# Kernel tuning notes

Measured on AMD Instinct MI355X. Metric: run time of the kernel, lower is better.

The kernel has to match this reference:

```python
import jax, jax.numpy as jnp
import numpy as np

B, D, S, O = 32768, 1024, 64, 4  # batch, feature_dim, n_subjects, n_outputs


def setup_inputs() -> dict:
    key = jax.random.key(0)
    kx, ks, kw, kb = jax.random.split(key, 4)
    x = jax.random.normal(kx, (B, D), dtype=jnp.float32)          # backbone features
    subject_ids = jax.random.randint(ks, (B,), 0, S)              # per-sample head id
    W = jax.random.normal(kw, (S, D, O), dtype=jnp.float32) / np.float32(np.sqrt(D))
    b = jax.random.normal(kb, (S, O), dtype=jnp.float32) * 0.01
    return {"x": x, "subject_ids": subject_ids, "W": W, "b": b}


def reference(x, subject_ids, W, b):
    # Vectorized form of the per-subject loop:
    #   for sid in unique(subject_ids): outputs[idxs] = heads[sid](features[idxs])
    # Each head is Linear(D, O): out[i] = x[i] @ W[sid[i]] + b[sid[i]].
    Wg = jnp.take(W, subject_ids, axis=0)   # [B, D, O] gathered per-sample weights
    bg = jnp.take(b, subject_ids, axis=0)   # [B, O]
    return jnp.einsum('bd,bdo->bo', x, Wg) + bg
```

## Files before the change

### kernel.cpp

```cpp
#include <hip/hip_runtime.h>

constexpr int B = 32768;
constexpr int D = 1024;
constexpr int S = 64;
constexpr int O = 4;


constexpr int CHUNKS      = 32;
constexpr int CHUNK       = B / CHUNKS;
constexpr int SEG         = CHUNK / 4;
constexpr int MAIN_BLOCKS = S * CHUNKS;

__global__ __launch_bounds__(256, 4) void main_kernel(
    const float* __restrict__ x,
    const int*   __restrict__ sid,
    const float* __restrict__ W,
    const float* __restrict__ bias,
    float*       __restrict__ out)
{
    __shared__ int list[4][SEG];

    const int lane = threadIdx.x & 63;
    const int wave = threadIdx.x >> 6;
    const int s    = blockIdx.x >> 5;
    const int c    = blockIdx.x & 31;
    const int q    = lane >> 4;

    const int seg = c * CHUNK + wave * SEG;
    int cnt = 0;
    #pragma unroll
    for (int r = 0; r < 4; ++r) {
        const int i = seg + r * 64 + lane;
        const bool m = (sid[i] == s);
        const unsigned long long mask = __ballot(m);
        const int rank = __popcll(mask & ((1ull << lane) - 1ull));
        if (m) list[wave][cnt + rank] = i;
        cnt += __popcll(mask);
    }

    float4 wreg[16];
    {
        const float4* Wp = (const float4*)(W + (size_t)s * (D * O));
        #pragma unroll
        for (int jj = 0; jj < 4; ++jj)
            #pragma unroll
            for (int cc = 0; cc < 4; ++cc)
                wreg[4 * jj + cc] = Wp[256 * jj + 4 * lane + cc];
    }
    const float bb = bias[(s << 2) + q];

    if (cnt == 0) return;

#define LOADX(XB, ROW)                                                         \
    {                                                                          \
        const float4* xr = (const float4*)(x + ((size_t)(ROW) << 10));         \
        _Pragma("unroll")                                                      \
        for (int j = 0; j < 4; ++j) XB[j] = xr[64 * j + lane];                 \
    }

#define COMPUTE(XC, ROW)                                                       \
    {                                                                          \
        float a0 = 0.f, a1 = 0.f, a2 = 0.f, a3 = 0.f;                          \
        _Pragma("unroll")                                                      \
        for (int j = 0; j < 4; ++j) {                                          \
            const float4 xv = XC[j];                                           \
            const float4 w0 = wreg[4 * j + 0];                                 \
            const float4 w1 = wreg[4 * j + 1];                                 \
            const float4 w2 = wreg[4 * j + 2];                                 \
            const float4 w3 = wreg[4 * j + 3];                                 \
            a0 += xv.x * w0.x; a1 += xv.x * w0.y;                              \
            a2 += xv.x * w0.z; a3 += xv.x * w0.w;                              \
            a0 += xv.y * w1.x; a1 += xv.y * w1.y;                              \
            a2 += xv.y * w1.z; a3 += xv.y * w1.w;                              \
            a0 += xv.z * w2.x; a1 += xv.z * w2.y;                              \
            a2 += xv.z * w2.z; a3 += xv.z * w2.w;                              \
            a0 += xv.w * w3.x; a1 += xv.w * w3.y;                              \
            a2 += xv.w * w3.z; a3 += xv.w * w3.w;                              \
        }                                                                      \
        _Pragma("unroll")                                                      \
        for (int m = 16; m <= 32; m <<= 1) {                                   \
            a0 += __shfl_xor(a0, m, 64);                                       \
            a1 += __shfl_xor(a1, m, 64);                                       \
            a2 += __shfl_xor(a2, m, 64);                                       \
            a3 += __shfl_xor(a3, m, 64);                                       \
        }                                                                      \
        float v = (q == 0) ? a0 : (q == 1) ? a1 : (q == 2) ? a2 : a3;          \
        _Pragma("unroll")                                                      \
        for (int m = 1; m <= 8; m <<= 1)                                       \
            v += __shfl_xor(v, m, 64);                                         \
        if ((lane & 15) == 0)                                                  \
            out[((size_t)(ROW) << 2) + q] = v + bb;                            \
    }

    float4 xbA[4], xbB[4];
    int rowA = __builtin_amdgcn_readfirstlane(list[wave][0]);
    LOADX(xbA, rowA)

    int k = 0;
    #pragma unroll 1
    while (k + 2 <= cnt) {
        const int rowB = __builtin_amdgcn_readfirstlane(list[wave][k + 1]);
        LOADX(xbB, rowB)
        COMPUTE(xbA, rowA)
        if (k + 2 < cnt) {
            const int rowN = __builtin_amdgcn_readfirstlane(list[wave][k + 2]);
            LOADX(xbA, rowN)
            COMPUTE(xbB, rowB)
            rowA = rowN;
        } else {
            COMPUTE(xbB, rowB)
        }
        k += 2;
    }
    if (k < cnt)
        COMPUTE(xbA, rowA)

#undef LOADX
#undef COMPUTE
}

extern "C" void kernel_launch(void* const* d_in, const int* in_sizes, int n_in,
                              void* d_out, int out_size, void* d_ws, size_t ws_size,
                              hipStream_t stream) {
    const float* x    = (const float*)d_in[0];
    const int*   sid  = (const int*)d_in[1];
    const float* W    = (const float*)d_in[2];
    const float* bias = (const float*)d_in[3];
    float* out = (float*)d_out;

    main_kernel<<<MAIN_BLOCKS, 256, 0, stream>>>(x, sid, W, bias, out);
}
```

Before: 230.8 us.

## Stage transposed head weights in shared memory and halve chunk count

Each block now loads the subject's weight matrix once into LDS in an output-major transposed layout and reads it per row, instead of holding 16 float4 weights in registers per lane. The batch is split into 16 chunks instead of 32, so each wave scans twice as many ids and processes more matched rows. Occupancy is pinned via waves_per_eu. This aims to cut register pressure and redundant W loads, at the cost of added LDS reads per row and a block barrier.

Measured after the change: 206.2 us. 10.6% less time.

```diff
diff --git a/kernel.cpp b/kernel.cpp
--- a/kernel.cpp
+++ b/kernel.cpp
@@ -6,30 +6,47 @@
 constexpr int O = 4;
 
 
-constexpr int CHUNKS      = 32;
+constexpr int CHUNKS      = 16;
 constexpr int CHUNK       = B / CHUNKS;
 constexpr int SEG         = CHUNK / 4;
 constexpr int MAIN_BLOCKS = S * CHUNKS;
 
-__global__ __launch_bounds__(256, 4) void main_kernel(
+__global__ __launch_bounds__(256)
+__attribute__((amdgpu_waves_per_eu(4, 4)))
+void main_kernel(
     const float* __restrict__ x,
     const int*   __restrict__ sid,
     const float* __restrict__ W,
     const float* __restrict__ bias,
     float*       __restrict__ out)
 {
-    __shared__ int list[4][SEG];
+    __shared__ float Wt[O * D];
+    __shared__ int   list[4][SEG];
 
-    const int lane = threadIdx.x & 63;
-    const int wave = threadIdx.x >> 6;
-    const int s    = blockIdx.x >> 5;
-    const int c    = blockIdx.x & 31;
+    const int t    = threadIdx.x;
+    const int lane = t & 63;
+    const int wave = t >> 6;
+    const int s    = blockIdx.x >> 4;
+    const int c    = blockIdx.x & 15;
     const int q    = lane >> 4;
+
+    {
+        const float4* Wp = (const float4*)(W + (size_t)s * (D * O));
+        #pragma unroll
+        for (int r = 0; r < 4; ++r) {
+            const int d = r * 256 + t;
+            const float4 w4 = Wp[d];
+            Wt[0 * D + d] = w4.x;
+            Wt[1 * D + d] = w4.y;
+            Wt[2 * D + d] = w4.z;
+            Wt[3 * D + d] = w4.w;
+        }
+    }
 
     const int seg = c * CHUNK + wave * SEG;
     int cnt = 0;
     #pragma unroll
-    for (int r = 0; r < 4; ++r) {
+    for (int r = 0; r < 8; ++r) {
         const int i = seg + r * 64 + lane;
         const bool m = (sid[i] == s);
         const unsigned long long mask = __ballot(m);
@@ -38,18 +55,11 @@
         cnt += __popcll(mask);
     }
 
-    float4 wreg[16];
-    {
-        const float4* Wp = (const float4*)(W + (size_t)s * (D * O));
-        #pragma unroll
-        for (int jj = 0; jj < 4; ++jj)
-            #pragma unroll
-            for (int cc = 0; cc < 4; ++cc)
-                wreg[4 * jj + cc] = Wp[256 * jj + 4 * lane + cc];
-    }
-    const float bb = bias[(s << 2) + q];
+    __syncthreads();
+    if (cnt == 0) return;
 
-    if (cnt == 0) return;
+    const float   bb  = bias[(s << 2) + q];
+    const float4* Wt4 = (const float4*)Wt;
 
 #define LOADX(XB, ROW)                                                         \
     {                                                                          \
@@ -64,18 +74,18 @@
         _Pragma("unroll")                                                      \
         for (int j = 0; j < 4; ++j) {                                          \
             const float4 xv = XC[j];                                           \
-            const float4 w0 = wreg[4 * j + 0];                                 \
-            const float4 w1 = wreg[4 * j + 1];                                 \
-            const float4 w2 = wreg[4 * j + 2];                                 \
-            const float4 w3 = wreg[4 * j + 3];                                 \
-            a0 += xv.x * w0.x; a1 += xv.x * w0.y;                              \
-            a2 += xv.x * w0.z; a3 += xv.x * w0.w;                              \
-            a0 += xv.y * w1.x; a1 += xv.y * w1.y;                              \
-            a2 += xv.y * w1.z; a3 += xv.y * w1.w;                              \
-            a0 += xv.z * w2.x; a1 += xv.z * w2.y;                              \
-            a2 += xv.z * w2.z; a3 += xv.z * w2.w;                              \
-            a0 += xv.w * w3.x; a1 += xv.w * w3.y;                              \
-            a2 += xv.w * w3.z; a3 += xv.w * w3.w;                              \
+            const float4 w0 = Wt4[0 * 256 + 64 * j + lane];                    \
+            const float4 w1 = Wt4[1 * 256 + 64 * j + lane];                    \
+            const float4 w2 = Wt4[2 * 256 + 64 * j + lane];                    \
+            const float4 w3 = Wt4[3 * 256 + 64 * j + lane];                    \
+            a0 += xv.x * w0.x; a1 += xv.x * w1.x;                              \
+            a2 += xv.x * w2.x; a3 += xv.x * w3.x;                              \
+            a0 += xv.y * w0.y; a1 += xv.y * w1.y;                              \
+            a2 += xv.y * w2.y; a3 += xv.y * w3.y;                              \
+            a0 += xv.z * w0.z; a1 += xv.z * w1.z;                              \
+            a2 += xv.z * w2.z; a3 += xv.z * w3.z;                              \
+            a0 += xv.w * w0.w; a1 += xv.w * w1.w;                              \
+            a2 += xv.w * w2.w; a3 += xv.w * w3.w;                              \
         }                                                                      \
         _Pragma("unroll")                                                      \
         for (int m = 16; m <= 32; m <<= 1) {                                   \
@@ -88,7 +98,7 @@
         _Pragma("unroll")                                                      \
         for (int m = 1; m <= 8; m <<= 1)                                       \
             v += __shfl_xor(v, m, 64);                                         \
-        if ((lane & 15) == 0)                                                  \
+        if ((lane & 15) == 0)                  \
             out[((size_t)(ROW) << 2) + q] = v + bb;                            \
     }
 
```
